# Optimization experiments

Hardware: AMD Instinct MI355X
Metric: run time of the kernel (lower is better)

## Reference

```python
import jax, jax.numpy as jnp
import numpy as np

T, H = 8192, 512
MC, MD = 4096, 4096
N_ENT = 128
MAX_DIST = 600  # POSITION_EMBEDDING_IN_DIM


def _make_spans(k, m, t):
    ks, kl = jax.random.split(k)
    starts = jax.random.randint(ks, (m,), 0, t - 8, dtype=jnp.int64)
    lens = jax.random.randint(kl, (m,), 0, 8, dtype=jnp.int64)
    return jnp.stack([starts, starts + lens], axis=1)  # inclusive [start, end], end < T


def setup_inputs() -> dict:
    key = jax.random.key(0)
    k = jax.random.split(key, 8)
    h = jax.random.normal(k[0], (T, H), dtype=jnp.float32)
    chem_spans = _make_spans(k[1], MC, T)
    dis_spans = _make_spans(k[2], MD, T)
    # deterministic entity assignment guarantees every entity has mentions
    chem_ent = jnp.arange(MC, dtype=jnp.int64) % N_ENT
    dis_ent = jnp.arange(MD, dtype=jnp.int64) % N_ENT
    s = 0.05
    return {
        "h": h,
        "chem_spans": chem_spans, "chem_ent": chem_ent,
        "dis_spans": dis_spans, "dis_ent": dis_ent,
        "Wc": jax.random.normal(k[3], (H, 100), jnp.float32) * s,
        "bc": jnp.zeros((100,), jnp.float32),
        "Wd": jax.random.normal(k[4], (H, 100), jnp.float32) * s,
        "bd": jnp.zeros((100,), jnp.float32),
        "Wemb": jax.random.normal(k[5], (MAX_DIST, 50), jnp.float32),
        "Ws": jax.random.normal(k[6], (250, 2), jnp.float32) * s,
        "bs": jnp.zeros((2,), jnp.float32),
        "n_chem": N_ENT,
        "n_dis": N_ENT,
    }


def reference(h, chem_spans, chem_ent, dis_spans, dis_ent,
              Wc, bc, Wd, bd, Wemb, Ws, bs, n_chem, n_dis):
    # inclusive span sums via prefix sums: sum(h[s..e]) = csum[e+1] - csum[s]
    csum = jnp.concatenate([jnp.zeros((1, h.shape[1]), h.dtype), jnp.cumsum(h, axis=0)], axis=0)
    c_sum = csum[chem_spans[:, 1] + 1] - csum[chem_spans[:, 0]]  # [MC, H]
    d_sum = csum[dis_spans[:, 1] + 1] - csum[dis_spans[:, 0]]    # [MD, H]
    c_feat = jnp.tanh(c_sum @ Wc + bc)  # [MC, 100]
    d_feat = jnp.tanh(d_sum @ Wd + bd)  # [MD, 100]
    # score Dense over concat(c, d, emb) decomposed linearly (same math)
    sc_c = c_feat @ Ws[:100]            # [MC, 2]
    sc_d = d_feat @ Ws[100:200]         # [MD, 2]
    emb_sc = Wemb @ Ws[200:250]         # [600, 2] pre-contracted embedding scores
    dist = jnp.minimum(jnp.abs(chem_spans[:, 0][:, None] - dis_spans[:, 0][None, :]),
                       MAX_DIST - 1)    # [MC, MD]
    pair = sc_c[:, None, :] + sc_d[None, :, :] + emb_sc[dist] + bs  # [MC, MD, 2]
    # running max over all mention pairs of each (chem entity, disease entity)
    pair_ids = (chem_ent[:, None] * n_dis + dis_ent[None, :]).reshape(-1)
    neg = jnp.full((n_chem * n_dis, 2), -jnp.inf, dtype=pair.dtype)
    ent_max = neg.at[pair_ids].max(pair.reshape(-1, 2))
    return jax.nn.softmax(ent_max, axis=-1).reshape(n_chem, n_dis, 2)
```

## Files before the change

### kernel.cpp

```cpp
#include <hip/hip_runtime.h>
#include <math.h>
#include <limits.h>

#define H_DIM  512
#define NFEAT  100
#define NPAD   112
#define NT     7
#define MAXD   600
#define MAXE   2048
#define SB     16
#define CHK    64
#define DCH    64

#define NEG_ENC 0x007FFFFFu

typedef __attribute__((ext_vector_type(8))) short short8v;
typedef __attribute__((ext_vector_type(4))) float f32x4;

__device__ __forceinline__ unsigned enc_f(float f){
    unsigned u = __float_as_uint(f);
    return (u & 0x80000000u) ? ~u : (u | 0x80000000u);
}
__device__ __forceinline__ float dec_f(unsigned e){
    unsigned u = (e & 0x80000000u) ? (e ^ 0x80000000u) : ~e;
    return __uint_as_float(u);
}
__device__ __forceinline__ unsigned short f2bf(float f){
    unsigned x = __float_as_uint(f);
    return (unsigned short)((x + 0x7fffu + ((x >> 16) & 1u)) >> 16);
}

__global__ __launch_bounds__(256) void prep_kernel(
    const float* __restrict__ h,
    const float* __restrict__ Wemb, const float* __restrict__ Ws,
    const float* __restrict__ bs,
    const float* __restrict__ Wc,   const float* __restrict__ Wd,
    const int* __restrict__ cent, const int* __restrict__ dent,
    const int* __restrict__ ncp,  const int* __restrict__ ndp,
    float* __restrict__ emb2, unsigned* __restrict__ gent, int gent_n,
    unsigned short* __restrict__ Wt, unsigned short* __restrict__ hbf,
    int* __restrict__ ghist,
    int MCv, int MDv, int TT, int off_e, int off_w, int off_h)
{
    const int tid = threadIdx.x;
    const int bid = blockIdx.x;

    if (bid < 32){
        __shared__ int hist[MAXE];
        const int side = bid >> 4;
        const int b    = bid & 15;
        const int ne   = side ? *ndp : *ncp;
        if (ne > MAXE) return;
        const int* ent = side ? dent : cent;
        const int  M   = side ? MDv : MCv;
        const int chunk = (M + SB - 1) / SB;
        const int i0 = b * chunk, i1 = min(M, i0 + chunk);
        for (int e = tid; e < ne; e += 256) hist[e] = 0;
        __syncthreads();
        for (int i = i0 + tid; i < i1; i += 256) atomicAdd(&hist[ent[i]], 1);
        __syncthreads();
        int* gh = ghist + (side*SB + b) * MAXE;
        for (int e = tid; e < ne; e += 256) gh[e] = hist[e];
    } else if (bid < off_e){
        int i = (bid - 32) * 256 + tid;
        if (i < gent_n) gent[i] = NEG_ENC;
    } else if (bid < off_w){
        int d = (bid - off_e) * 256 + tid;
        if (d < MAXD){
            float a0 = bs[0], a1 = bs[1];
            #pragma unroll 5
            for (int q = 0; q < 50; ++q){
                float w = Wemb[d*50 + q];
                a0 += w * Ws[(200+q)*2 + 0];
                a1 += w * Ws[(200+q)*2 + 1];
            }
            emb2[d*2 + 0] = a0;
            emb2[d*2 + 1] = a1;
        }
    } else if (bid < off_h){
        const int base = (bid - off_w) * 4096;
        #pragma unroll
        for (int ii = 0; ii < 16; ++ii){
            int e = base + tid + 256*ii;
            if (e < 2*NPAD*H_DIM){
                int side = e / (NPAD*H_DIM);
                int rem  = e - side*(NPAD*H_DIM);
                int n    = rem / H_DIM;
                int k    = rem - n*H_DIM;
                const float* W = side ? Wd : Wc;
                Wt[e] = (n < NFEAT) ? f2bf(W[k*NFEAT + n]) : (unsigned short)0;
            }
        }
    } else {
        const long base = (long)(bid - off_h) * 2048 + (long)tid * 8;
        if (base < (long)TT * H_DIM){
            float4 lo = *reinterpret_cast<const float4*>(h + base);
            float4 hi = *reinterpret_cast<const float4*>(h + base + 4);
            union { unsigned short us[8]; uint4 v; } o;
            o.us[0]=f2bf(lo.x); o.us[1]=f2bf(lo.y); o.us[2]=f2bf(lo.z); o.us[3]=f2bf(lo.w);
            o.us[4]=f2bf(hi.x); o.us[5]=f2bf(hi.y); o.us[6]=f2bf(hi.z); o.us[7]=f2bf(hi.w);
            *reinterpret_cast<uint4*>(hbf + base) = o.v;
        }
    }
}

__global__ __launch_bounds__(128) void hw_gemm(
    const unsigned short* __restrict__ hbf,
    const unsigned short* __restrict__ Wt,
    float* __restrict__ HW, int mt_total, int TT,
    const int* __restrict__ cent, const int* __restrict__ dent,
    const int* __restrict__ ncp,  const int* __restrict__ ndp,
    const int* __restrict__ cspans, const int* __restrict__ dspans,
    const int* __restrict__ ghist,
    int4* __restrict__ csorted, int4* __restrict__ dsorted,
    int MCv, int MDv)
{
    __shared__ int s_tot[MAXE];
    __shared__ int s_cur[MAXE];
    __shared__ int s_wsum[2];

    if ((int)blockIdx.x >= mt_total){
        const int sb   = blockIdx.x - mt_total;
        const int side = sb >> 4;
        const int b    = sb & 15;
        const int tid  = threadIdx.x;
        const int ne   = side ? *ndp : *ncp;
        const int* ent = side ? dent : cent;
        const int* spans = side ? dspans : cspans;
        int4* out      = side ? dsorted : csorted;
        const int M    = side ? MDv : MCv;
        const int chunk = (M + SB - 1) / SB;
        const int i0 = b * chunk, i1 = min(M, i0 + chunk);

        if (ne <= MAXE){
            const int* gh = ghist + side*SB*MAXE;
            for (int e = tid; e < ne; e += 128){
                int pre = 0, tot = 0;
                #pragma unroll
                for (int bb = 0; bb < SB; ++bb){
                    int v = gh[bb*MAXE + e];
                    tot += v;
                    pre += (bb < b) ? v : 0;
                }
                s_tot[e] = tot;
                s_cur[e] = pre;
            }
            __syncthreads();
            const int per = (ne + 127) / 128;
            const int lo = min(tid*per, ne), hi = min(lo + per, ne);
            int sum = 0;
            for (int j = lo; j < hi; ++j) sum += s_tot[j];
            const int lane = tid & 63, w = tid >> 6;
            int x = sum;
            #pragma unroll
            for (int k = 1; k < 64; k <<= 1){
                int y = __shfl_up(x, k);
                if (lane >= k) x += y;
            }
            int excl = x - sum;
            if (lane == 63) s_wsum[w] = x;
            __syncthreads();
            if (w == 1) excl += s_wsum[0];
            int run = excl;
            for (int j = lo; j < hi; ++j){
                int t = s_tot[j];
                s_cur[j] += run;
                run += t;
            }
            __syncthreads();
            for (int i = i0 + tid; i < i1; i += 128){
                int e = ent[i];
                int pos = atomicAdd(&s_cur[e], 1);
                out[pos] = make_int4(spans[i*2], e, i, 0);
            }
        } else {
            for (int i = i0 + tid; i < i1; i += 128)
                out[i] = make_int4(spans[i*2], ent[i], i, 0);
        }
        return;
    }

    const int wid  = blockIdx.x * 2 + (threadIdx.x >> 6);
    const int lane = threadIdx.x & 63;
    const int side = wid / mt_total;
    const int mt   = wid - side * mt_total;
    if (side > 1) return;

    const unsigned short* A = hbf + (size_t)(mt*16 + (lane & 15)) * H_DIM + (lane >> 4) * 8;
    const unsigned short* B = Wt + (size_t)side * NPAD * H_DIM
                                 + (size_t)(lane & 15) * H_DIM + (lane >> 4) * 8;
    float* D = HW + (size_t)side * TT * NPAD;

    f32x4 acc[NT];
    #pragma unroll
    for (int nt = 0; nt < NT; ++nt) acc[nt] = (f32x4){0.f,0.f,0.f,0.f};

    #pragma unroll 4
    for (int ks = 0; ks < H_DIM/32; ++ks){
        short8v a = *reinterpret_cast<const short8v*>(A + ks*32);
        #pragma unroll
        for (int nt = 0; nt < NT; ++nt){
            short8v b = *reinterpret_cast<const short8v*>(B + (size_t)nt*16*H_DIM + ks*32);
            acc[nt] = __builtin_amdgcn_mfma_f32_16x16x32_bf16(a, b, acc[nt], 0, 0, 0);
        }
    }

    const int col = lane & 15;
    const int r0  = (lane >> 4) * 4;
    #pragma unroll
    for (int nt = 0; nt < NT; ++nt){
        #pragma unroll
        for (int r = 0; r < 4; ++r)
            D[(size_t)(mt*16 + r0 + r) * NPAD + nt*16 + col] = acc[nt][r];
    }
}

__global__ __launch_bounds__(128) void feat_kernel(
    const float* __restrict__ HW,
    const int* __restrict__ cspans, const int* __restrict__ dspans,
    const float* __restrict__ bc,   const float* __restrict__ bd,
    const float* __restrict__ Ws,
    float* __restrict__ sc_c, float* __restrict__ sc_d,
    int MCv, int MDv, int TT)
{
    __shared__ float red[2][2];
    const int bidx = blockIdx.x;
    const bool isd = (bidx >= MCv);
    const int  m   = isd ? (bidx - MCv) : bidx;
    const int* spans = isd ? dspans : cspans;
    const float* b   = isd ? bd : bc;
    const int  wsoff = isd ? NFEAT : 0;

    const int tid = threadIdx.x;
    const int s   = spans[m*2];
    const int len = spans[m*2 + 1] - s;

    float p0 = 0.f, p1 = 0.f;
    if (tid < NFEAT){
        const float* base = HW + (isd ? (size_t)TT*NPAD : 0) + (size_t)s*NPAD + tid;
        float v[8];
        #pragma unroll
        for (int r = 0; r < 8; ++r) v[r] = base[(size_t)r*NPAD];
        float val = 0.f;
        #pragma unroll
        for (int r = 0; r < 8; ++r) val += (r <= len) ? v[r] : 0.f;
        float f = tanhf(val + b[tid]);
        p0 = f * Ws[(wsoff + tid)*2 + 0];
        p1 = f * Ws[(wsoff + tid)*2 + 1];
    }
    #pragma unroll
    for (int k = 32; k >= 1; k >>= 1){
        p0 += __shfl_down(p0, k);
        p1 += __shfl_down(p1, k);
    }
    if ((tid & 63) == 0){ red[tid>>6][0] = p0; red[tid>>6][1] = p1; }
    __syncthreads();
    if (tid == 0){
        float* sc = isd ? sc_d : sc_c;
        sc[m*2 + 0] = red[0][0] + red[1][0];
        sc[m*2 + 1] = red[0][1] + red[1][1];
    }
}

__device__ __forceinline__ void flush_run(
    float s0, float s1, int ce, int de, int nd, bool head,
    const bool okk[6], unsigned* __restrict__ gent)
{
    float a0 = s0, a1 = s1;
    #pragma unroll
    for (int k = 0; k < 6; ++k){
        float b0 = __shfl_down(a0, 1 << k);
        float b1 = __shfl_down(a1, 1 << k);
        if (okk[k]){ a0 = fmaxf(a0, b0); a1 = fmaxf(a1, b1); }
    }
    if (head && ce != INT_MAX){
        atomicMax(&gent[(ce*nd + de)*2 + 0], enc_f(a0));
        atomicMax(&gent[(ce*nd + de)*2 + 1], enc_f(a1));
    }
}

__global__ __launch_bounds__(256) void pair_kernel(
    const int4* __restrict__ csorted, const int4* __restrict__ dsorted,
    const float* __restrict__ sc_c,   const float* __restrict__ sc_d,
    const float* __restrict__ emb2,   const int* __restrict__ ndp,
    unsigned* __restrict__ gent, int MCv, int MDv)
{
    __shared__ float2 s_e[MAXD];
    __shared__ int4   s_d[CHK];

    const int tid  = threadIdx.x;
    const int lane = tid & 63;
    const int nd   = *ndp;

    const float2* e2 = (const float2*)emb2;
    for (int i = tid; i < MAXD; i += 256) s_e[i] = e2[i];

    int   cs = 0, ce = INT_MAX;
    float c0 = 0.f, c1 = 0.f;
    {
        int ci = blockIdx.x * 256 + tid;
        if (ci < MCv){
            int4 r = csorted[ci];
            cs = r.x; ce = r.y;
            const float2 sc = *reinterpret_cast<const float2*>(&sc_c[2*r.z]);
            c0 = sc.x; c1 = sc.y;
        }
    }
    int ceprev = __shfl_up(ce, 1);
    const bool head = (lane == 0) || (ceprev != ce);
    bool okk[6];
    #pragma unroll
    for (int k = 0; k < 6; ++k) okk[k] = (__shfl_down(ce, 1 << k) == ce);

    for (int cb = blockIdx.y; cb * CHK < MDv; cb += DCH){
        const int dbase = cb * CHK;
        const int n = min(CHK, MDv - dbase);
        __syncthreads();
        for (int i = tid; i < n; i += 256){
            int4 r = dsorted[dbase + i];
            const float2 sd = *reinterpret_cast<const float2*>(&sc_d[2*r.z]);
            s_d[i] = make_int4(r.x, r.y, __float_as_int(sd.x), __float_as_int(sd.y));
        }
        __syncthreads();

        int   cur_de = s_d[0].y;
        float s0 = -INFINITY, s1 = -INFINITY;
        for (int j = 0; j < n; ++j){
            int4 dj = s_d[j];
            if (dj.y != cur_de){
                flush_run(s0, s1, ce, cur_de, nd, head, okk, gent);
                cur_de = dj.y; s0 = -INFINITY; s1 = -INFINITY;
            }
            int dd = cs - dj.x; dd = dd < 0 ? -dd : dd;
            dd = dd < (MAXD-1) ? dd : (MAXD-1);
            float2 e = s_e[dd];
            s0 = fmaxf(s0, c0 + __int_as_float(dj.z) + e.x);
            s1 = fmaxf(s1, c1 + __int_as_float(dj.w) + e.y);
        }
        flush_run(s0, s1, ce, cur_de, nd, head, okk, gent);
    }
}

__global__ void softmax_kernel(const unsigned* __restrict__ gent,
                               float* __restrict__ out, int npairs){
    int p = blockIdx.x * blockDim.x + threadIdx.x;
    if (p < npairs){
        float a = dec_f(gent[p*2 + 0]);
        float b = dec_f(gent[p*2 + 1]);
        float m = fmaxf(a, b);
        float ea = expf(a - m), eb = expf(b - m);
        float inv = 1.f / (ea + eb);
        out[p*2 + 0] = ea * inv;
        out[p*2 + 1] = eb * inv;
    }
}

extern "C" void kernel_launch(void* const* d_in, const int* in_sizes, int n_in,
                              void* d_out, int out_size, void* d_ws, size_t ws_size,
                              hipStream_t stream)
{
    const float* h      = (const float*)d_in[0];
    const int*   cspans = (const int*)  d_in[1];
    const int*   centp  = (const int*)  d_in[2];
    const int*   dspans = (const int*)  d_in[3];
    const int*   dentp  = (const int*)  d_in[4];
    const float* Wc     = (const float*)d_in[5];
    const float* bc     = (const float*)d_in[6];
    const float* Wd     = (const float*)d_in[7];
    const float* bd     = (const float*)d_in[8];
    const float* Wemb   = (const float*)d_in[9];
    const float* Ws     = (const float*)d_in[10];
    const float* bs     = (const float*)d_in[11];
    const int*   ncp    = (const int*)  d_in[12];
    const int*   ndp    = (const int*)  d_in[13];

    const int MCv    = in_sizes[1] / 2;
    const int MDv    = in_sizes[3] / 2;
    const int TT     = in_sizes[0] / H_DIM;
    const int npairs = out_size / 2;

    float*    wsf    = (float*)d_ws;
    float*    emb2   = wsf;
    float*    sc_c   = wsf + 1280;
    float*    sc_d   = sc_c + (size_t)MCv * 2;
    unsigned* gent   = (unsigned*)(sc_d + (size_t)MDv * 2);
    int4*     csorted= (int4*)(gent + out_size);
    int4*     dsorted= csorted + MCv;
    unsigned short* hbf = (unsigned short*)(dsorted + MDv);
    unsigned short* Wt  = hbf + (size_t)TT * H_DIM;
    int*      ghist  = (int*)(Wt + 2 * NPAD * H_DIM);
    float*    HW     = (float*)(ghist + 2 * SB * MAXE);

    const int gb    = (out_size + 255) / 256;
    const int eb    = (MAXD + 255) / 256;
    const int wb    = (2*NPAD*H_DIM + 4095) / 4096;
    const int hb    = (int)(((long)TT * H_DIM + 2047) / 2048);
    const int off_e = 32 + gb;
    const int off_w = off_e + eb;
    const int off_h = off_w + wb;

    hipLaunchKernelGGL(prep_kernel, dim3(off_h + hb), dim3(256), 0, stream,
                       h, Wemb, Ws, bs, Wc, Wd, centp, dentp, ncp, ndp,
                       emb2, gent, out_size, Wt, hbf, ghist,
                       MCv, MDv, TT, off_e, off_w, off_h);

    const int mt_total = TT / 16;
    hipLaunchKernelGGL(hw_gemm, dim3(mt_total + 32), dim3(128), 0, stream,
                       hbf, Wt, HW, mt_total, TT,
                       centp, dentp, ncp, ndp, cspans, dspans,
                       ghist, csorted, dsorted, MCv, MDv);

    hipLaunchKernelGGL(feat_kernel, dim3(MCv + MDv), dim3(128), 0, stream,
                       HW, cspans, dspans, bc, bd, Ws, sc_c, sc_d, MCv, MDv, TT);

    hipLaunchKernelGGL(pair_kernel, dim3((MCv + 255)/256, DCH), dim3(256), 0, stream,
                       csorted, dsorted, sc_c, sc_d, emb2, ndp, gent, MCv, MDv);

    hipLaunchKernelGGL(softmax_kernel, dim3((npairs + 255)/256), dim3(256), 0, stream,
                       gent, (float*)d_out, npairs);
}
```

Baseline: 134.3 us.

## Sum spans before GEMM and fuse feature tanh/score into GEMM kernel

Instead of converting all of h to bf16 and multiplying every token row by W, the prep kernel now sums the fp32 rows of each mention span and writes one bf16 row per mention. The GEMM then runs over mention rows, split-K across four waves reduced through shared memory. Bias, tanh and the Ws projection are applied in the GEMM epilogue, which removes the separate feat kernel and the HW intermediate buffer. This cuts GEMM work and one launch, but span sums are now rounded to bf16 after summation rather than before, and it reads up to 8 rows per mention from h.

```diff
diff --git a/kernel.cpp b/kernel.cpp
--- a/kernel.cpp
+++ b/kernel.cpp
@@ -6,6 +6,7 @@
 #define NFEAT  100
 #define NPAD   112
 #define NT     7
+#define KW     4
 #define MAXD   600
 #define MAXE   2048
 #define SB     16
@@ -37,10 +38,11 @@
     const float* __restrict__ Wc,   const float* __restrict__ Wd,
     const int* __restrict__ cent, const int* __restrict__ dent,
     const int* __restrict__ ncp,  const int* __restrict__ ndp,
+    const int* __restrict__ cspans, const int* __restrict__ dspans,
     float* __restrict__ emb2, unsigned* __restrict__ gent, int gent_n,
-    unsigned short* __restrict__ Wt, unsigned short* __restrict__ hbf,
+    unsigned short* __restrict__ Wt, unsigned short* __restrict__ S,
     int* __restrict__ ghist,
-    int MCv, int MDv, int TT, int off_e, int off_w, int off_h)
+    int MCv, int MDv, int MCs16, int Rtot, int off_e, int off_w, int off_h)
 {
     const int tid = threadIdx.x;
     const int bid = blockIdx.x;
@@ -92,38 +94,67 @@
             }
         }
     } else {
-        const long base = (long)(bid - off_h) * 2048 + (long)tid * 8;
-        if (base < (long)TT * H_DIM){
-            float4 lo = *reinterpret_cast<const float4*>(h + base);
-            float4 hi = *reinterpret_cast<const float4*>(h + base + 4);
+        const int row = (bid - off_h) * 4 + (tid >> 6);
+        if (row < Rtot){
+            const int side = (row >= MCs16);
+            const int ml   = side ? (row - MCs16) : row;
+            const int M    = side ? MDv : MCv;
+            const int col0 = (tid & 63) * 8;
+            float a0=0.f,a1=0.f,a2=0.f,a3=0.f,a4=0.f,a5=0.f,a6=0.f,a7=0.f;
+            if (ml < M){
+                const int* spans = side ? dspans : cspans;
+                const int s   = spans[ml*2];
+                const int len = spans[ml*2 + 1] - s;
+                const float* hp = h + (size_t)s * H_DIM + col0;
+                float4 v0[8], v1[8];
+                #pragma unroll
+                for (int r = 0; r < 8; ++r){
+                    v0[r] = *reinterpret_cast<const float4*>(hp + (size_t)r*H_DIM);
+                    v1[r] = *reinterpret_cast<const float4*>(hp + (size_t)r*H_DIM + 4);
+                }
+                #pragma unroll
+                for (int r = 0; r < 8; ++r){
+                    if (r <= len){
+                        a0+=v0[r].x; a1+=v0[r].y; a2+=v0[r].z; a3+=v0[r].w;
+                        a4+=v1[r].x; a5+=v1[r].y; a6+=v1[r].z; a7+=v1[r].w;
+                    }
+                }
+            }
             union { unsigned short us[8]; uint4 v; } o;
-            o.us[0]=f2bf(lo.x); o.us[1]=f2bf(lo.y); o.us[2]=f2bf(lo.z); o.us[3]=f2bf(lo.w);
-            o.us[4]=f2bf(hi.x); o.us[5]=f2bf(hi.y); o.us[6]=f2bf(hi.z); o.us[7]=f2bf(hi.w);
-            *reinterpret_cast<uint4*>(hbf + base) = o.v;
-        }
-    }
-}
-
-__global__ __launch_bounds__(128) void hw_gemm(
-    const unsigned short* __restrict__ hbf,
+            o.us[0]=f2bf(a0); o.us[1]=f2bf(a1); o.us[2]=f2bf(a2); o.us[3]=f2bf(a3);
+            o.us[4]=f2bf(a4); o.us[5]=f2bf(a5); o.us[6]=f2bf(a6); o.us[7]=f2bf(a7);
+            *reinterpret_cast<uint4*>(S + (size_t)row * H_DIM + col0) = o.v;
+        }
+    }
+}
+
+__global__ __launch_bounds__(256) void gemm_feat(
+    const unsigned short* __restrict__ S,
     const unsigned short* __restrict__ Wt,
-    float* __restrict__ HW, int mt_total, int TT,
+    const float* __restrict__ bc, const float* __restrict__ bd,
+    const float* __restrict__ Ws,
+    float* __restrict__ sc_c, float* __restrict__ sc_d,
     const int* __restrict__ cent, const int* __restrict__ dent,
     const int* __restrict__ ncp,  const int* __restrict__ ndp,
     const int* __restrict__ cspans, const int* __restrict__ dspans,
     const int* __restrict__ ghist,
     int4* __restrict__ csorted, int4* __restrict__ dsorted,
-    int MCv, int MDv)
+    int mtc, int mtd, int MCv, int MDv, int MCs16)
 {
-    __shared__ int s_tot[MAXE];
-    __shared__ int s_cur[MAXE];
-    __shared__ int s_wsum[2];
-
-    if ((int)blockIdx.x >= mt_total){
-        const int sb   = blockIdx.x - mt_total;
+    __shared__ float s_acc[KW-1][NT*4][64];
+    __shared__ int   s_tot[MAXE];
+    __shared__ int   s_cur[MAXE];
+    __shared__ int   s_wsum[4];
+
+    const int tid  = threadIdx.x;
+    const int lane = tid & 63;
+    const int w    = tid >> 6;
+    const int bid  = blockIdx.x;
+
+    if (bid >= mtc + mtd){
+        const int sb   = bid - (mtc + mtd);
         const int side = sb >> 4;
         const int b    = sb & 15;
-        const int tid  = threadIdx.x;
         const int ne   = side ? *ndp : *ncp;
         const int* ent = side ? dent : cent;
         const int* spans = side ? dspans : cspans;
@@ -134,7 +165,7 @@
 
         if (ne <= MAXE){
             const int* gh = ghist + side*SB*MAXE;
-            for (int e = tid; e < ne; e += 128){
+            for (int e = tid; e < ne; e += 256){
                 int pre = 0, tot = 0;
                 #pragma unroll
                 for (int bb = 0; bb < SB; ++bb){
@@ -146,11 +177,10 @@
                 s_cur[e] = pre;
             }
             __syncthreads();
-            const int per = (ne + 127) / 128;
+            const int per = (ne + 255) / 256;
             const int lo = min(tid*per, ne), hi = min(lo + per, ne);
             int sum = 0;
             for (int j = lo; j < hi; ++j) sum += s_tot[j];
-            const int lane = tid & 63, w = tid >> 6;
             int x = sum;
             #pragma unroll
             for (int k = 1; k < 64; k <<= 1){
@@ -160,43 +190,41 @@
             int excl = x - sum;
             if (lane == 63) s_wsum[w] = x;
             __syncthreads();
-            if (w == 1) excl += s_wsum[0];
+            for (int ww = 0; ww < w; ++ww) excl += s_wsum[ww];
             int run = excl;
             for (int j = lo; j < hi; ++j){
-                int t = s_tot[j];
                 s_cur[j] += run;
-                run += t;
+                run += s_tot[j];
             }
             __syncthreads();
-            for (int i = i0 + tid; i < i1; i += 128){
+            for (int i = i0 + tid; i < i1; i += 256){
                 int e = ent[i];
                 int pos = atomicAdd(&s_cur[e], 1);
                 out[pos] = make_int4(spans[i*2], e, i, 0);
             }
         } else {
-            for (int i = i0 + tid; i < i1; i += 128)
+            for (int i = i0 + tid; i < i1; i += 256)
                 out[i] = make_int4(spans[i*2], ent[i], i, 0);
         }
         return;
     }
 
-    const int wid  = blockIdx.x * 2 + (threadIdx.x >> 6);
-    const int lane = threadIdx.x & 63;
-    const int side = wid / mt_total;
-    const int mt   = wid - side * mt_total;
-    if (side > 1) return;
-
-    const unsigned short* A = hbf + (size_t)(mt*16 + (lane & 15)) * H_DIM + (lane >> 4) * 8;
+    const int side = (bid >= mtc);
+    const int mt   = side ? (bid - mtc) : bid;
+    const int row0 = (side ? MCs16 : 0) + mt*16;
+
+    const unsigned short* A = S + (size_t)(row0 + (lane & 15)) * H_DIM
+                                + (lane >> 4) * 8 + w * 4 * 32;
     const unsigned short* B = Wt + (size_t)side * NPAD * H_DIM
-                                 + (size_t)(lane & 15) * H_DIM + (lane >> 4) * 8;
-    float* D = HW + (size_t)side * TT * NPAD;
+                                 + (size_t)(lane & 15) * H_DIM
+                                 + (lane >> 4) * 8 + w * 4 * 32;
 
     f32x4 acc[NT];
     #pragma unroll
     for (int nt = 0; nt < NT; ++nt) acc[nt] = (f32x4){0.f,0.f,0.f,0.f};
 
-    #pragma unroll 4
-    for (int ks = 0; ks < H_DIM/32; ++ks){
+    #pragma unroll
+    for (int ks = 0; ks < 4; ++ks){
         short8v a = *reinterpret_cast<const short8v*>(A + ks*32);
         #pragma unroll
         for (int nt = 0; nt < NT; ++nt){
@@ -205,60 +233,58 @@
         }
     }
 
-    const int col = lane & 15;
-    const int r0  = (lane >> 4) * 4;
-    #pragma unroll
-    for (int nt = 0; nt < NT; ++nt){
-        #pragma unroll
-        for (int r = 0; r < 4; ++r)
-            D[(size_t)(mt*16 + r0 + r) * NPAD + nt*16 + col] = acc[nt][r];
-    }
-}
-
-__global__ __launch_bounds__(128) void feat_kernel(
-    const float* __restrict__ HW,
-    const int* __restrict__ cspans, const int* __restrict__ dspans,
-    const float* __restrict__ bc,   const float* __restrict__ bd,
-    const float* __restrict__ Ws,
-    float* __restrict__ sc_c, float* __restrict__ sc_d,
-    int MCv, int MDv, int TT)
-{
-    __shared__ float red[2][2];
-    const int bidx = blockIdx.x;
-    const bool isd = (bidx >= MCv);
-    const int  m   = isd ? (bidx - MCv) : bidx;
-    const int* spans = isd ? dspans : cspans;
-    const float* b   = isd ? bd : bc;
-    const int  wsoff = isd ? NFEAT : 0;
-
-    const int tid = threadIdx.x;
-    const int s   = spans[m*2];
-    const int len = spans[m*2 + 1] - s;
-
-    float p0 = 0.f, p1 = 0.f;
-    if (tid < NFEAT){
-        const float* base = HW + (isd ? (size_t)TT*NPAD : 0) + (size_t)s*NPAD + tid;
-        float v[8];
-        #pragma unroll
-        for (int r = 0; r < 8; ++r) v[r] = base[(size_t)r*NPAD];
-        float val = 0.f;
-        #pragma unroll
-        for (int r = 0; r < 8; ++r) val += (r <= len) ? v[r] : 0.f;
-        float f = tanhf(val + b[tid]);
-        p0 = f * Ws[(wsoff + tid)*2 + 0];
-        p1 = f * Ws[(wsoff + tid)*2 + 1];
-    }
-    #pragma unroll
-    for (int k = 32; k >= 1; k >>= 1){
-        p0 += __shfl_down(p0, k);
-        p1 += __shfl_down(p1, k);
-    }
-    if ((tid & 63) == 0){ red[tid>>6][0] = p0; red[tid>>6][1] = p1; }
+    if (w > 0){
+        #pragma unroll
+        for (int nt = 0; nt < NT; ++nt)
+            #pragma unroll
+            for (int r = 0; r < 4; ++r)
+                s_acc[w-1][nt*4 + r][lane] = acc[nt][r];
+    }
     __syncthreads();
-    if (tid == 0){
-        float* sc = isd ? sc_d : sc_c;
-        sc[m*2 + 0] = red[0][0] + red[1][0];
-        sc[m*2 + 1] = red[0][1] + red[1][1];
+    if (w == 0){
+        #pragma unroll
+        for (int nt = 0; nt < NT; ++nt)
+            #pragma unroll
+            for (int r = 0; r < 4; ++r)
+                acc[nt][r] += s_acc[0][nt*4+r][lane]
+                            + s_acc[1][nt*4+r][lane]
+                            + s_acc[2][nt*4+r][lane];
+
+        const float* bvec = side ? bd : bc;
+        const int    wsoff = side ? NFEAT : 0;
+        const int    nb    = lane & 15;
+        float bb[NT], w0[NT], w1[NT];
+        #pragma unroll
+        for (int nt = 0; nt < NT; ++nt){
+            int n = nt*16 + nb;
+            bool v = (n < NFEAT);
+            bb[nt] = v ? bvec[n] : 0.f;
+            w0[nt] = v ? Ws[(wsoff + n)*2 + 0] : 0.f;
+            w1[nt] = v ? Ws[(wsoff + n)*2 + 1] : 0.f;
+        }
+        const int ml0 = mt*16 + (lane >> 4)*4;
+        const int M   = side ? MDv : MCv;
+        float* sc     = side ? sc_d : sc_c;
+        #pragma unroll
+        for (int r = 0; r < 4; ++r){
+            float p0 = 0.f, p1 = 0.f;
+            #pragma unroll
+            for (int nt = 0; nt < NT; ++nt){
+                float f = tanhf(acc[nt][r] + bb[nt]);
+                p0 += f * w0[nt];
+                p1 += f * w1[nt];
+            }
+            #pragma unroll
+            for (int k = 1; k < 16; k <<= 1){
+                p0 += __shfl_xor(p0, k);
+                p1 += __shfl_xor(p1, k);
+            }
+            int ml = ml0 + r;
+            if (nb == 0 && ml < M){
+                sc[ml*2 + 0] = p0;
+                sc[ml*2 + 1] = p1;
+            }
+        }
     }
 }
 
@@ -376,8 +402,12 @@
 
     const int MCv    = in_sizes[1] / 2;
     const int MDv    = in_sizes[3] / 2;
-    const int TT     = in_sizes[0] / H_DIM;
     const int npairs = out_size / 2;
+
+    const int mtc   = (MCv + 15) / 16;
+    const int mtd   = (MDv + 15) / 16;
+    const int MCs16 = mtc * 16;
+    const int Rtot  = (mtc + mtd) * 16;
 
     float*    wsf    = (float*)d_ws;
     float*    emb2   = wsf;
@@ -386,32 +416,27 @@
     unsigned* gent   = (unsigned*)(sc_d + (size_t)MDv * 2);
     int4*     csorted= (int4*)(gent + out_size);
     int4*     dsorted= csorted + MCv;
-    unsigned short* hbf = (unsigned short*)(dsorted + MDv);
-    unsigned short* Wt  = hbf + (size_t)TT * H_DIM;
+    unsigned short* S  = (unsigned short*)(dsorted + MDv);
+    unsigned short* Wt = S + (size_t)Rtot * H_DIM;
     int*      ghist  = (int*)(Wt + 2 * NPAD * H_DIM);
-    float*    HW     = (float*)(ghist + 2 * SB * MAXE);
 
     const int gb    = (out_size + 255) / 256;
     const int eb    = (MAXD + 255) / 256;
     const int wb    = (2*NPAD*H_DIM + 4095) / 4096;
-    const int hb    = (int)(((long)TT * H_DIM + 2047) / 2048);
+    const int sb    = (Rtot + 3) / 4;
     const int off_e = 32 + gb;
     const int off_w = off_e + eb;
     const int off_h = off_w + wb;
 
-    hipLaunchKernelGGL(prep_kernel, dim3(off_h + hb), dim3(256), 0, stream,
+    hipLaunchKernelGGL(prep_kernel, dim3(off_h + sb), dim3(256), 0, stream,
                        h, Wemb, Ws, bs, Wc, Wd, centp, dentp, ncp, ndp,
-                       emb2, gent, out_size, Wt, hbf, ghist,
-                       MCv, MDv, TT, off_e, off_w, off_h);
-
-    const int mt_total = TT / 16;
-    hipLaunchKernelGGL(hw_gemm, dim3(mt_total + 32), dim3(128), 0, stream,
-                       hbf, Wt, HW, mt_total, TT,
+                       cspans, dspans, emb2, gent, out_size, Wt, S, ghist,
+                       MCv, MDv, MCs16, Rtot, off_e, off_w, off_h);
+
+    hipLaunchKernelGGL(gemm_feat, dim3(mtc + mtd + 32), dim3(256), 0, stream,
+                       S, Wt, bc, bd, Ws, sc_c, sc_d,
                        centp, dentp, ncp, ndp, cspans, dspans,
-                       ghist, csorted, dsorted, MCv, MDv);
-
-    hipLaunchKernelGGL(feat_kernel, dim3(MCv + MDv), dim3(128), 0, stream,
-                       HW, cspans, dspans, bc, bd, Ws, sc_c, sc_d, MCv, MDv, TT);
+                       ghist, csorted, dsorted, mtc, mtd, MCv, MDv, MCs16);
 
     hipLaunchKernelGGL(pair_kernel, dim3((MCv + 255)/256, DCH), dim3(256), 0, stream,
                        csorted, dsorted, sc_c, sc_d, emb2, ndp, gent, MCv, MDv);
```

After: 131.7 us. -2.0%, faster.
